# Performance work log

Hardware: AMD Instinct MI355X
Metric: run time of the kernel (lower is better)

## Reference

```python
import jax, jax.numpy as jnp
import numpy as np

N_AGENTS = 16      # args['num_agents']
BATCH = 8192       # args['n_rollout_threads'] -> number of independent graphs
OBS = 64           # cent_obs_shape[0] // n_nodes
HID = 128          # args['hidden_sizes'][0]
N_LAYERS = 2       # args['n_layers']
USE_RES = True     # args['use_res']


def _build_edges():
    # complete graph (no self loops) per graph, block-diagonal over BATCH graphs
    i, j = np.meshgrid(np.arange(N_AGENTS), np.arange(N_AGENTS), indexing='ij')
    m = i != j
    bs, bd = i[m], j[m]                      # [240]
    off = (np.arange(BATCH) * N_AGENTS)[:, None]
    src = (bs[None, :] + off).ravel().astype(np.int32)  # [BATCH*240]
    dst = (bd[None, :] + off).ravel().astype(np.int32)
    return src, dst


def setup_inputs() -> dict:
    key = jax.random.key(0)
    ks = jax.random.split(key, 5)
    N = BATCH * N_AGENTS
    src, dst = _build_edges()
    return {
        'cent_obs': jax.random.normal(ks[0], (N, OBS), jnp.float32),
        'w_emb': jax.random.normal(ks[1], (OBS, HID), jnp.float32) / np.sqrt(OBS).astype(np.float32),
        'b_emb': jnp.zeros((HID,), jnp.float32),
        'w_gcn': jax.random.normal(ks[2], (N_LAYERS, HID, HID), jnp.float32) / np.sqrt(HID).astype(np.float32),
        'b_gcn': jnp.zeros((N_LAYERS, HID), jnp.float32),
        'w_fc1': jax.random.normal(ks[3], (HID, 1), jnp.float32) / np.sqrt(HID).astype(np.float32),
        'b_fc1': jnp.zeros((1,), jnp.float32),
        'edge_src': jnp.asarray(src),
        'edge_dst': jnp.asarray(dst),
    }


def reference(cent_obs, w_emb, b_emb, w_gcn, b_gcn, w_fc1, b_fc1, edge_src, edge_dst):
    N = cent_obs.shape[0]
    # embedding_in
    x = cent_obs @ w_emb + b_emb                           # [N, HID]
    # GCNConv normalization with added self-loops (PyG default, sym norm)
    loop = jnp.arange(N, dtype=edge_src.dtype)
    src = jnp.concatenate([edge_src, loop])
    dst = jnp.concatenate([edge_dst, loop])
    deg = jax.ops.segment_sum(jnp.ones_like(dst, dtype=x.dtype), dst, num_segments=N)
    inv_sqrt = jax.lax.rsqrt(deg)
    norm = (inv_sqrt[src] * inv_sqrt[dst])[:, None]        # [E+N, 1]
    for l in range(N_LAYERS):
        h = x @ w_gcn[l]                                   # linear transform
        agg = jax.ops.segment_sum(h[src] * norm, dst, num_segments=N) + b_gcn[l]
        x = jnp.tanh(agg + x if USE_RES else agg)
    value = x @ w_fc1 + b_fc1                              # [N, 1]
    value = value.reshape(BATCH, -1)                       # [BATCH, n_nodes]
    return value.mean(axis=1).reshape(-1, 1)               # [BATCH, 1]
```

## Files before the change

kernel.cpp:

```cpp
#include <hip/hip_runtime.h>


#define N_GRAPHS 8192
#define BLOCK    256
#define NBLOCKS  (N_GRAPHS / 8)

typedef __attribute__((ext_vector_type(8)))  short short8;
typedef __attribute__((ext_vector_type(4)))  float floatx4;
typedef __attribute__((ext_vector_type(16))) float floatx16;

#define MFMA16(a, b, c) __builtin_amdgcn_mfma_f32_16x16x32_bf16((a), (b), (c), 0, 0, 0)
#define MFMA32(a, b, c) __builtin_amdgcn_mfma_f32_32x32x16_bf16((a), (b), (c), 0, 0, 0)

#define EMB_LO   1024
#define GCN_BASE 2048
#define GCN_LO   2048

#define K2LOG2E 2.885390081777927f

#if __has_builtin(__builtin_amdgcn_exp2f)
#define EXP2R(x) __builtin_amdgcn_exp2f(x)
#else
#define EXP2R(x) __expf(0.6931471805599453f * (x))
#endif
#if __has_builtin(__builtin_amdgcn_rcpf)
#define RCPF(x) __builtin_amdgcn_rcpf(x)
#else
#define RCPF(x) __fdividef(1.0f, (x))
#endif

union fragu { unsigned int u[4]; short8 s8; };

__device__ __forceinline__ unsigned fbits(float x) {
  union { float f; unsigned u; } v; v.f = x; return v.u;
}
__device__ __forceinline__ float bitsf(unsigned u) {
  union { float f; unsigned u; } v; v.u = u; return v.f;
}
__device__ __forceinline__ void bsplit(float x, short& hi, short& lo) {
  unsigned hb = fbits(x) & 0xFFFF0000u;
  hi = (short)(hb >> 16);
  lo = (short)(fbits(x - bitsf(hb)) >> 16);
}
__device__ __forceinline__ unsigned hpack(unsigned b_odd, unsigned b_even) {
  return __builtin_amdgcn_perm(b_odd, b_even, 0x07060302u);
}
__device__ __forceinline__ void mk_frags(float4 a, float4 b, short8& hi, short8& lo) {
  fragu H, L;
  H.u[0] = hpack(fbits(a.y), fbits(a.x));
  H.u[1] = hpack(fbits(a.w), fbits(a.z));
  H.u[2] = hpack(fbits(b.y), fbits(b.x));
  H.u[3] = hpack(fbits(b.w), fbits(b.z));
  float l0 = a.x - bitsf(fbits(a.x) & 0xFFFF0000u);
  float l1 = a.y - bitsf(fbits(a.y) & 0xFFFF0000u);
  float l2 = a.z - bitsf(fbits(a.z) & 0xFFFF0000u);
  float l3 = a.w - bitsf(fbits(a.w) & 0xFFFF0000u);
  float l4 = b.x - bitsf(fbits(b.x) & 0xFFFF0000u);
  float l5 = b.y - bitsf(fbits(b.y) & 0xFFFF0000u);
  float l6 = b.z - bitsf(fbits(b.z) & 0xFFFF0000u);
  float l7 = b.w - bitsf(fbits(b.w) & 0xFFFF0000u);
  L.u[0] = hpack(fbits(l1), fbits(l0));
  L.u[1] = hpack(fbits(l3), fbits(l2));
  L.u[2] = hpack(fbits(l5), fbits(l4));
  L.u[3] = hpack(fbits(l7), fbits(l6));
  hi = H.s8; lo = L.s8;
}
__device__ __forceinline__ float fast_tanh2(float x, float zc) {
  float e = EXP2R(fmaf(x, K2LOG2E, zc));
  return fmaf(-2.0f, RCPF(e + 1.0f), 1.0f);
}

__global__ __launch_bounds__(BLOCK) void gcn_prep(
    const float* __restrict__ w_emb, const float* __restrict__ w_gcn,
    unsigned short* __restrict__ wsS)
{
  int idx = blockIdx.x * BLOCK + threadIdx.x;
  if (idx >= 40960) return;
  int f = idx >> 3, j = idx & 7;
  const float* src;
  int hi_f, lo_f;
  if (f < 1024) {
    int ks = f >> 8, t = (f >> 6) & 3, L = f & 63;
    int k0 = ks * 16 + (L >> 5) * 8;
    int n  = t * 32 + (L & 31);
    src = w_emb + k0 * 128 + n;
    hi_f = f; lo_f = f + EMB_LO;
  } else {
    int f2 = f - 1024;
    int l = f2 >> 11, r = f2 & 2047;
    int kc = r >> 9, nt = (r >> 6) & 7, L = r & 63;
    int k0 = kc * 32 + (L >> 4) * 8;
    int n  = nt * 16 + (L & 15);
    src = w_gcn + l * 16384 + k0 * 128 + n;
    hi_f = GCN_BASE + l * 4096 + r; lo_f = hi_f + GCN_LO;
  }
  short h, l_;
  bsplit(src[j * 128], h, l_);
  wsS[hi_f * 8 + j] = (unsigned short)h;
  wsS[lo_f * 8 + j] = (unsigned short)l_;
}

__global__ __launch_bounds__(BLOCK, 4) void gcn_main(
    const float* __restrict__ obs,
    const float* __restrict__ b_emb,
    const float* __restrict__ b_gcn,
    const float* __restrict__ w_fc1,
    const float* __restrict__ b_fc1,
    const short8* __restrict__ tab,
    float* __restrict__ out)
{
  __shared__ short sA[2 * 4 * 16 * 40];
  __shared__ float sH[8][129];
  __shared__ short8 sE[1024];

  const int tid = threadIdx.x;
  const int w   = tid >> 6;
  const int L   = tid & 63;
  const int m32 = L & 31;
  const int kh  = L >> 5;
  const int c16 = L & 15;
  const int q   = L >> 4;
  const int gw  = blockIdx.x * 8 + 2 * w;

  const float* op = obs + (gw * 16 + m32) * 64 + kh * 8;
  float4 oa0 = *(const float4*)(op);
  float4 oa1 = *(const float4*)(op + 4);

  floatx16 x[4];
  #pragma unroll
  for (int t = 0; t < 4; ++t) {
    float b = b_emb[t * 32 + m32];
    #pragma unroll
    for (int r = 0; r < 16; ++r) x[t][r] = b;
  }

#if __has_builtin(__builtin_amdgcn_global_load_lds)
  #pragma unroll
  for (int i = 0; i < 4; ++i) {
    __builtin_amdgcn_global_load_lds(
        (const __attribute__((address_space(1))) unsigned int*)(tab + tid + 256 * i),
        (__attribute__((address_space(3))) unsigned int*)&sE[tid + 256 * i],
        16, 0, 0);
  }
#else
  #pragma unroll
  for (int i = 0; i < 4; ++i) sE[tid + 256 * i] = tab[tid + 256 * i];
#endif

  {
    unsigned int* za = (unsigned int*)sA;
    #pragma unroll
    for (int jz = 0; jz < 5; ++jz) {
      int i   = tid + 256 * jz;
      int tb_ = i / 160;
      int rm  = i - tb_ * 160;
      int rr  = rm / 20, cw = rm - rr * 20;
      za[tb_ * 320 + (rr + 8) * 20 + cw] = 0;
    }
  }
  __syncthreads();

  short8 nbh = sE[L];
  short8 nbl = tab[EMB_LO + L];
  #pragma unroll
  for (int s = 0; s < 4; ++s) {
    short8 ah, al;
    mk_frags(oa0, oa1, ah, al);
    if (s < 3) {
      oa0 = *(const float4*)(op + (s + 1) * 16);
      oa1 = *(const float4*)(op + (s + 1) * 16 + 4);
    }
    #pragma unroll
    for (int t = 0; t < 4; ++t) {
      short8 bh = nbh, bl = nbl;
      if (s * 4 + t < 15) {
        int nidx = (s * 4 + t + 1) * 64 + L;
        nbh = sE[nidx];
        nbl = tab[nidx + EMB_LO];
      }
      x[t] = MFMA32(ah, bh, x[t]);
      x[t] = MFMA32(al, bh, x[t]);
      x[t] = MFMA32(ah, bl, x[t]);
    }
  }

  #pragma unroll 1
  for (int l = 0; l < 2; ++l) {
    const short8* t0 = tab + GCN_BASE + l * 4096 + (2 * w) * 64 + L;
    const short8* t1 = t0 + 64;
    short8 cbh0 = t0[0], cbh1 = t1[0];
    short8 cbl0 = t0[GCN_LO], cbl1 = t1[GCN_LO];

    #pragma unroll
    for (int t = 0; t < 4; ++t) {
      float s0 = x[t][0], s1 = x[t][8];
      #pragma unroll
      for (int r = 1; r < 8; ++r) { s0 += x[t][r]; s1 += x[t][r + 8]; }
      s0 += __shfl_xor(s0, 32);
      s1 += __shfl_xor(s1, 32);
      s0 *= 0.0625f; s1 *= 0.0625f;
      #pragma unroll
      for (int rr = 0; rr < 2; ++rr) {
        float v = rr ? s1 : s0;
        unsigned hb = fbits(v) & 0xFFFF0000u;
        unsigned vb = (kh == 0) ? hb : fbits(v - bitsf(hb));
        unsigned nb = (unsigned)__shfl_xor((int)vb, 1);
        unsigned pw = hpack(nb, vb);
        if ((m32 & 1) == 0) {
          int si = kh * 2560 + t * 640 + (2 * w + rr) * 40
                 + (m32 >> 3) * 8 + (m32 & 7);
          *(unsigned int*)&sA[si] = pw;
        }
      }
    }
    __syncthreads();

    floatx4 h0 = {0.f, 0.f, 0.f, 0.f};
    floatx4 h1 = {0.f, 0.f, 0.f, 0.f};
    #pragma unroll
    for (int kc = 0; kc < 4; ++kc) {
      short8 ah = *(const short8*)&sA[kc * 640 + c16 * 40 + q * 8];
      short8 al = *(const short8*)&sA[2560 + kc * 640 + c16 * 40 + q * 8];
      short8 nbh0, nbh1, nbl0, nbl1;
      if (kc < 3) {
        nbh0 = t0[(kc + 1) * 512];
        nbh1 = t1[(kc + 1) * 512];
        nbl0 = t0[(kc + 1) * 512 + GCN_LO];
        nbl1 = t1[(kc + 1) * 512 + GCN_LO];
      }
      h0 = MFMA16(ah, cbh0, h0); h1 = MFMA16(ah, cbh1, h1);
      h0 = MFMA16(al, cbh0, h0); h1 = MFMA16(al, cbh1, h1);
      h0 = MFMA16(ah, cbl0, h0); h1 = MFMA16(ah, cbl1, h1);
      cbh0 = nbh0; cbh1 = nbh1; cbl0 = nbl0; cbl1 = nbl1;
    }

    float bg0 = b_gcn[l * 128 + m32];
    float bg1 = b_gcn[l * 128 + 32 + m32];
    float bg2 = b_gcn[l * 128 + 64 + m32];
    float bg3 = b_gcn[l * 128 + 96 + m32];

    if (q < 2) {
      #pragma unroll
      for (int r = 0; r < 4; ++r) {
        sH[q * 4 + r][(2 * w) * 16 + c16]     = h0[r];
        sH[q * 4 + r][(2 * w + 1) * 16 + c16] = h1[r];
      }
    }
    __syncthreads();

    float bg[4] = {bg0, bg1, bg2, bg3};
    #pragma unroll
    for (int t = 0; t < 4; ++t) {
      float zcA = (sH[2 * w][t * 32 + m32] + bg[t]) * K2LOG2E;
      float zcB = (sH[2 * w + 1][t * 32 + m32] + bg[t]) * K2LOG2E;
      #pragma unroll
      for (int r = 0; r < 8; ++r) {
        x[t][r]     = fast_tanh2(x[t][r], zcA);
        x[t][r + 8] = fast_tanh2(x[t][r + 8], zcB);
      }
    }
  }

  float wf0 = w_fc1[m32];
  float wf1 = w_fc1[32 + m32];
  float wf2 = w_fc1[64 + m32];
  float wf3 = w_fc1[96 + m32];
  float wf[4] = {wf0, wf1, wf2, wf3};
  float vA = 0.f, vB = 0.f;
  #pragma unroll
  for (int t = 0; t < 4; ++t) {
    float sA_ = 0.f, sB_ = 0.f;
    #pragma unroll
    for (int r = 0; r < 8; ++r) { sA_ += x[t][r]; sB_ += x[t][r + 8]; }
    vA = fmaf(sA_, wf[t], vA);
    vB = fmaf(sB_, wf[t], vB);
  }
  #pragma unroll
  for (int d = 32; d >= 1; d >>= 1) {
    vA += __shfl_xor(vA, d);
    vB += __shfl_xor(vB, d);
  }
  if (L == 0) {
    float bf = b_fc1[0];
    out[gw]     = vA * 0.0625f + bf;
    out[gw + 1] = vB * 0.0625f + bf;
  }
}

extern "C" void kernel_launch(void* const* d_in, const int* in_sizes, int n_in,
                              void* d_out, int out_size, void* d_ws, size_t ws_size,
                              hipStream_t stream) {
  const float* obs    = (const float*)d_in[0];
  const float* w_emb  = (const float*)d_in[1];
  const float* b_emb  = (const float*)d_in[2];
  const float* w_gcn  = (const float*)d_in[3];
  const float* b_gcn  = (const float*)d_in[4];
  const float* w_fc1  = (const float*)d_in[5];
  const float* b_fc1  = (const float*)d_in[6];
  float* out = (float*)d_out;

  gcn_prep<<<160, BLOCK, 0, stream>>>(w_emb, w_gcn, (unsigned short*)d_ws);
  gcn_main<<<NBLOCKS, BLOCK, 0, stream>>>(obs, b_emb, b_gcn, w_fc1, b_fc1,
                                          (const short8*)d_ws, out);
}
```

Baseline: 108.7 us.

## Pack sixteen graphs per block to fill GCN MFMA tiles without padding

Doubles the block to 512 threads so each block handles sixteen graphs. The sixteen per-graph mean rows now fill the M dimension of the 16x16 MFMA tile used in the GCN layer matmul, so the zero-padded rows and the shared-memory zeroing that supported them go away. Each wave now computes one 16-column output tile instead of two, which halves the per-wave MFMA and weight-fragment work in the layer loop and spreads the weight-table load over more threads. The risks are fewer resident blocks per CU, larger barrier groups, and possible register-allocation changes under the new launch bounds.

```diff
diff --git a/kernel.cpp b/kernel.cpp
--- a/kernel.cpp
+++ b/kernel.cpp
@@ -2,8 +2,9 @@
 
 
 #define N_GRAPHS 8192
-#define BLOCK    256
-#define NBLOCKS  (N_GRAPHS / 8)
+#define BLOCKP   256
+#define BLOCKM   512
+#define NBLOCKS  (N_GRAPHS / 16)
 
 typedef __attribute__((ext_vector_type(8)))  short short8;
 typedef __attribute__((ext_vector_type(4)))  float floatx4;
@@ -70,11 +71,11 @@
   return fmaf(-2.0f, RCPF(e + 1.0f), 1.0f);
 }
 
-__global__ __launch_bounds__(BLOCK) void gcn_prep(
+__global__ __launch_bounds__(BLOCKP) void gcn_prep(
     const float* __restrict__ w_emb, const float* __restrict__ w_gcn,
     unsigned short* __restrict__ wsS)
 {
-  int idx = blockIdx.x * BLOCK + threadIdx.x;
+  int idx = blockIdx.x * BLOCKP + threadIdx.x;
   if (idx >= 40960) return;
   int f = idx >> 3, j = idx & 7;
   const float* src;
@@ -100,7 +101,7 @@
   wsS[lo_f * 8 + j] = (unsigned short)l_;
 }
 
-__global__ __launch_bounds__(BLOCK, 4) void gcn_main(
+__global__ __launch_bounds__(BLOCKM, 4) void gcn_main(
     const float* __restrict__ obs,
     const float* __restrict__ b_emb,
     const float* __restrict__ b_gcn,
@@ -110,7 +111,7 @@
     float* __restrict__ out)
 {
   __shared__ short sA[2 * 4 * 16 * 40];
-  __shared__ float sH[8][129];
+  __shared__ float sH[16][130];
   __shared__ short8 sE[1024];
 
   const int tid = threadIdx.x;
@@ -120,7 +121,7 @@
   const int kh  = L >> 5;
   const int c16 = L & 15;
   const int q   = L >> 4;
-  const int gw  = blockIdx.x * 8 + 2 * w;
+  const int gw  = blockIdx.x * 16 + 2 * w;
 
   const float* op = obs + (gw * 16 + m32) * 64 + kh * 8;
   float4 oa0 = *(const float4*)(op);
@@ -136,28 +137,16 @@
 
 #if __has_builtin(__builtin_amdgcn_global_load_lds)
   #pragma unroll
-  for (int i = 0; i < 4; ++i) {
+  for (int i = 0; i < 2; ++i) {
     __builtin_amdgcn_global_load_lds(
-        (const __attribute__((address_space(1))) unsigned int*)(tab + tid + 256 * i),
-        (__attribute__((address_space(3))) unsigned int*)&sE[tid + 256 * i],
+        (const __attribute__((address_space(1))) unsigned int*)(tab + tid + 512 * i),
+        (__attribute__((address_space(3))) unsigned int*)&sE[tid + 512 * i],
         16, 0, 0);
   }
 #else
   #pragma unroll
-  for (int i = 0; i < 4; ++i) sE[tid + 256 * i] = tab[tid + 256 * i];
+  for (int i = 0; i < 2; ++i) sE[tid + 512 * i] = tab[tid + 512 * i];
 #endif
-
-  {
-    unsigned int* za = (unsigned int*)sA;
-    #pragma unroll
-    for (int jz = 0; jz < 5; ++jz) {
-      int i   = tid + 256 * jz;
-      int tb_ = i / 160;
-      int rm  = i - tb_ * 160;
-      int rr  = rm / 20, cw = rm - rr * 20;
-      za[tb_ * 320 + (rr + 8) * 20 + cw] = 0;
-    }
-  }
   __syncthreads();
 
   short8 nbh = sE[L];
@@ -186,10 +175,9 @@
 
   #pragma unroll 1
   for (int l = 0; l < 2; ++l) {
-    const short8* t0 = tab + GCN_BASE + l * 4096 + (2 * w) * 64 + L;
-    const short8* t1 = t0 + 64;
-    short8 cbh0 = t0[0], cbh1 = t1[0];
-    short8 cbl0 = t0[GCN_LO], cbl1 = t1[GCN_LO];
+    const short8* t0 = tab + GCN_BASE + l * 4096 + w * 64 + L;
+    short8 cbh0 = t0[0];
+    short8 cbl0 = t0[GCN_LO];
 
     #pragma unroll
     for (int t = 0; t < 4; ++t) {
@@ -216,22 +204,19 @@
     __syncthreads();
 
     floatx4 h0 = {0.f, 0.f, 0.f, 0.f};
-    floatx4 h1 = {0.f, 0.f, 0.f, 0.f};
     #pragma unroll
     for (int kc = 0; kc < 4; ++kc) {
       short8 ah = *(const short8*)&sA[kc * 640 + c16 * 40 + q * 8];
       short8 al = *(const short8*)&sA[2560 + kc * 640 + c16 * 40 + q * 8];
-      short8 nbh0, nbh1, nbl0, nbl1;
+      short8 nbh0, nbl0;
       if (kc < 3) {
         nbh0 = t0[(kc + 1) * 512];
-        nbh1 = t1[(kc + 1) * 512];
         nbl0 = t0[(kc + 1) * 512 + GCN_LO];
-        nbl1 = t1[(kc + 1) * 512 + GCN_LO];
-      }
-      h0 = MFMA16(ah, cbh0, h0); h1 = MFMA16(ah, cbh1, h1);
-      h0 = MFMA16(al, cbh0, h0); h1 = MFMA16(al, cbh1, h1);
-      h0 = MFMA16(ah, cbl0, h0); h1 = MFMA16(ah, cbl1, h1);
-      cbh0 = nbh0; cbh1 = nbh1; cbl0 = nbl0; cbl1 = nbl1;
+      }
+      h0 = MFMA16(ah, cbh0, h0);
+      h0 = MFMA16(al, cbh0, h0);
+      h0 = MFMA16(ah, cbl0, h0);
+      cbh0 = nbh0; cbl0 = nbl0;
     }
 
     float bg0 = b_gcn[l * 128 + m32];
@@ -239,12 +224,9 @@
     float bg2 = b_gcn[l * 128 + 64 + m32];
     float bg3 = b_gcn[l * 128 + 96 + m32];
 
-    if (q < 2) {
-      #pragma unroll
-      for (int r = 0; r < 4; ++r) {
-        sH[q * 4 + r][(2 * w) * 16 + c16]     = h0[r];
-        sH[q * 4 + r][(2 * w + 1) * 16 + c16] = h1[r];
-      }
+    #pragma unroll
+    for (int r = 0; r < 4; ++r) {
+      sH[q * 4 + r][w * 16 + c16] = h0[r];
     }
     __syncthreads();
 
@@ -299,7 +281,7 @@
   const float* b_fc1  = (const float*)d_in[6];
   float* out = (float*)d_out;
 
-  gcn_prep<<<160, BLOCK, 0, stream>>>(w_emb, w_gcn, (unsigned short*)d_ws);
-  gcn_main<<<NBLOCKS, BLOCK, 0, stream>>>(obs, b_emb, b_gcn, w_fc1, b_fc1,
-                                          (const short8*)d_ws, out);
-}
+  gcn_prep<<<160, BLOCKP, 0, stream>>>(w_emb, w_gcn, (unsigned short*)d_ws);
+  gcn_main<<<NBLOCKS, BLOCKM, 0, stream>>>(obs, b_emb, b_gcn, w_fc1, b_fc1,
+                                           (const short8*)d_ws, out);
+}
```

Measured after the change: 108.2 us. About the same (-0.4%).
